# Optimization experiments

Measured on AMD Instinct MI355X. Metric: run time of the kernel, lower is better.

Reference implementation:

```python
import jax, jax.numpy as jnp
import numpy as np

EMBED = 128
HEADS = 8
PER_DIM = EMBED // HEADS


def setup_inputs() -> dict:
    key = jax.random.key(0)
    ks = jax.random.split(key, 8)
    N, T, C = 512, 32, EMBED
    values = jax.random.normal(ks[0], (N, T, C), dtype=jnp.float32)
    keys = jax.random.normal(ks[1], (N, T, C), dtype=jnp.float32)
    query = jax.random.normal(ks[2], (N, T, C), dtype=jnp.float32)
    s = 1.0 / np.sqrt(PER_DIM)
    Wq = jax.random.normal(ks[3], (PER_DIM, PER_DIM), dtype=jnp.float32) * s
    Wk = jax.random.normal(ks[4], (PER_DIM, PER_DIM), dtype=jnp.float32) * s
    Wv = jax.random.normal(ks[5], (PER_DIM, PER_DIM), dtype=jnp.float32) * s
    Wfc = jax.random.normal(ks[6], (C, C), dtype=jnp.float32) * (1.0 / np.sqrt(C))
    bfc = jax.random.normal(ks[7], (C,), dtype=jnp.float32) * 0.01
    return {"values": values, "keys": keys, "query": query, "heads": HEADS,
            "Wq": Wq, "Wk": Wk, "Wv": Wv, "Wfc": Wfc, "bfc": bfc}


def reference(values, keys, query, heads, Wq, Wk, Wv, Wfc, bfc):
    N, T, C = query.shape
    d = C // heads
    # Faithful to source bug: queries are built from `values`, not `query`.
    q = values.reshape(N, T, heads, d)
    k = keys.reshape(N, T, heads, d)
    v = values.reshape(N, T, heads, d)
    # nn.Linear (no bias): x @ W.T
    q = jnp.einsum('nthd,ed->nthe', q, Wq)
    k = jnp.einsum('nthd,ed->nthe', k, Wk)
    v = jnp.einsum('nthd,ed->nthe', v, Wv)
    # attention over the node axis: scores [q_node, k_node, t, h]
    attn = jnp.einsum('qthd,kthd->qkth', q, k)
    attention = jax.nn.softmax(attn / jnp.sqrt(jnp.float32(C)), axis=1)
    out = jnp.einsum('qkth,kthd->qthd', attention, v)
    out = out.reshape(N, T, C)
    out = jnp.einsum('ntc,ec->nte', out, Wfc) + bfc
    return out
```

## Files before the change

kernel.cpp:

```cpp
#include <hip/hip_runtime.h>

typedef __bf16 bf16x8 __attribute__((ext_vector_type(8)));
typedef float  f32x16 __attribute__((ext_vector_type(16)));

#define NN 512
#define TT 32
#define HH 8
#define CCH 128
#define RS (TT*CCH)
#define WS_U4_PER_TH 2048

__device__ __forceinline__ unsigned cvt_pk_bf16(float a, float b) {
    unsigned r;
    asm("v_cvt_pk_bf16_f32 %0, %1, %2" : "=v"(r) : "v"(a), "v"(b));
    return r;
}

__device__ __forceinline__ void permswap(unsigned& a, unsigned& b) {
    asm volatile("v_permlane32_swap_b32 %0, %1" : "+v"(a), "+v"(b));
}

__device__ __forceinline__ void split8(const float4 a, const float4 b, uint4& h, uint4& l) {
    const unsigned ax = __float_as_uint(a.x), ay = __float_as_uint(a.y);
    const unsigned az = __float_as_uint(a.z), aw = __float_as_uint(a.w);
    const unsigned bx = __float_as_uint(b.x), by = __float_as_uint(b.y);
    const unsigned bz = __float_as_uint(b.z), bw = __float_as_uint(b.w);
    h.x = (ay & 0xFFFF0000u) | (ax >> 16);
    h.y = (aw & 0xFFFF0000u) | (az >> 16);
    h.z = (by & 0xFFFF0000u) | (bx >> 16);
    h.w = (bw & 0xFFFF0000u) | (bz >> 16);
    const float lax = a.x - __uint_as_float(ax & 0xFFFF0000u);
    const float lay = a.y - __uint_as_float(ay & 0xFFFF0000u);
    const float laz = a.z - __uint_as_float(az & 0xFFFF0000u);
    const float law = a.w - __uint_as_float(aw & 0xFFFF0000u);
    const float lbx = b.x - __uint_as_float(bx & 0xFFFF0000u);
    const float lby = b.y - __uint_as_float(by & 0xFFFF0000u);
    const float lbz = b.z - __uint_as_float(bz & 0xFFFF0000u);
    const float lbw = b.w - __uint_as_float(bw & 0xFFFF0000u);
    l.x = cvt_pk_bf16(lax, lay);
    l.y = cvt_pk_bf16(laz, law);
    l.z = cvt_pk_bf16(lbx, lby);
    l.w = cvt_pk_bf16(lbz, lbw);
}

__global__ __launch_bounds__(256) void proj_kernel(
    const float* __restrict__ vals,
    const float* __restrict__ keys,
    const float* __restrict__ Wq,
    const float* __restrict__ Wk,
    const float* __restrict__ Wv,
    uint4* __restrict__ ws)
{
    __shared__ float wlds[512];
    __shared__ uint4 k2l[512];
    __shared__ uint4 vpl[512];

    const int tid  = threadIdx.x;
    const int bid  = blockIdx.x;
    const int th   = bid >> 1;
    const int half = bid & 1;
    const int t = th >> 3;
    const int h = th & 7;
    const size_t cb0 = (size_t)t*CCH + h*16;

    {
        const int d = tid >> 4, dp = tid & 15;
        float a = 0.f;
        #pragma unroll
        for (int e = 0; e < 16; ++e) a = fmaf(Wq[e*16+d], Wk[e*16+dp], a);
        wlds[tid]       = a * 0.12751744503131863f;
        wlds[256 + tid] = Wv[tid];
    }
    __syncthreads();

    const int n = half*256 + tid;
    const float* vrow = vals + (size_t)n*RS + cb0;
    const float* krow = keys + (size_t)n*RS + cb0;
    float kr[16], vr[16];
    #pragma unroll
    for (int i = 0; i < 16; i += 4) {
        *(float4*)&kr[i] = *(const float4*)(krow + i);
        *(float4*)&vr[i] = *(const float4*)(vrow + i);
    }
    float k2[16], vp[16];
    #pragma unroll
    for (int d = 0; d < 16; ++d) {
        const float4 m0 = *(const float4*)&wlds[d*16];
        const float4 m1 = *(const float4*)&wlds[d*16+4];
        const float4 m2 = *(const float4*)&wlds[d*16+8];
        const float4 m3 = *(const float4*)&wlds[d*16+12];
        const float4 w0 = *(const float4*)&wlds[256 + d*16];
        const float4 w1 = *(const float4*)&wlds[256 + d*16+4];
        const float4 w2 = *(const float4*)&wlds[256 + d*16+8];
        const float4 w3 = *(const float4*)&wlds[256 + d*16+12];
        k2[d] = kr[0]*m0.x + kr[1]*m0.y + kr[2]*m0.z + kr[3]*m0.w
              + kr[4]*m1.x + kr[5]*m1.y + kr[6]*m1.z + kr[7]*m1.w
              + kr[8]*m2.x + kr[9]*m2.y + kr[10]*m2.z + kr[11]*m2.w
              + kr[12]*m3.x + kr[13]*m3.y + kr[14]*m3.z + kr[15]*m3.w;
        vp[d] = vr[0]*w0.x + vr[1]*w0.y + vr[2]*w0.z + vr[3]*w0.w
              + vr[4]*w1.x + vr[5]*w1.y + vr[6]*w1.z + vr[7]*w1.w
              + vr[8]*w2.x + vr[9]*w2.y + vr[10]*w2.z + vr[11]*w2.w
              + vr[12]*w3.x + vr[13]*w3.y + vr[14]*w3.z + vr[15]*w3.w;
    }
    const int kt_loc = tid >> 5, r = tid & 31;
    uint4 lo4, hi4;
    lo4.x = cvt_pk_bf16(k2[0],k2[1]);   lo4.y = cvt_pk_bf16(k2[2],k2[3]);
    lo4.z = cvt_pk_bf16(k2[4],k2[5]);   lo4.w = cvt_pk_bf16(k2[6],k2[7]);
    hi4.x = cvt_pk_bf16(k2[8],k2[9]);   hi4.y = cvt_pk_bf16(k2[10],k2[11]);
    hi4.z = cvt_pk_bf16(k2[12],k2[13]); hi4.w = cvt_pk_bf16(k2[14],k2[15]);
    k2l[kt_loc*64 + r]      = lo4;
    k2l[kt_loc*64 + r + 32] = hi4;
    {
        unsigned short* vph = (unsigned short*)vpl;
        const int f_loc = kt_loc*2 + (r >> 4);
        const int lg = (r >> 3) & 1;
        const int ii = r & 7;
        #pragma unroll
        for (int e = 0; e < 16; ++e)
            vph[(size_t)(f_loc*32 + lg*16 + e)*8 + ii] =
                (unsigned short)(cvt_pk_bf16(vp[e], vp[e]) & 0xffffu);
    }
    __syncthreads();

    uint4* dk = ws + (size_t)th*WS_U4_PER_TH + half*512;
    uint4* dv = ws + (size_t)th*WS_U4_PER_TH + 1024 + half*512;
    #pragma unroll
    for (int i = 0; i < 2; ++i) {
        dk[i*256 + tid] = k2l[i*256 + tid];
        dv[i*256 + tid] = vpl[i*256 + tid];
    }
}

__global__ __launch_bounds__(256, 4) void attn_mfma(
    const float* __restrict__ vals,
    const uint4* __restrict__ ws,
    float* __restrict__ obuf)
{
    __shared__ uint4 k2f[1024];
    __shared__ uint4 vpfc[1024];
    __shared__ uint4 dummy[32];

    const int tid  = threadIdx.x;
    const int lane = tid & 63;
    const int wv   = tid >> 6;
    const int bid  = blockIdx.x;
    const int th   = bid & 255;
    const int qq   = bid >> 8;
    const int t = th >> 3;
    const int h = th & 7;
    const size_t cb0 = (size_t)t*CCH + h*16;

    const int qr = lane & 31;
    const int dh = (lane >> 5) * 8;

    const int nq = qq*128 + wv*32 + qr;
    const float* qp = vals + (size_t)nq*RS + cb0 + dh;
    const float4 qa = *(const float4*)qp;
    const float4 qb = *(const float4*)(qp + 4);

    const uint4* src = ws + (size_t)th*WS_U4_PER_TH;
    #pragma unroll
    for (int i = 0; i < 4; ++i) k2f[i*256 + tid]  = src[i*256 + tid];
    #pragma unroll
    for (int i = 0; i < 4; ++i) vpfc[i*256 + tid] = src[1024 + i*256 + tid];
    if (tid < 32) {
        const unsigned pv = (tid == 0 || tid == 16) ? 0x3F803F80u : 0u;
        dummy[tid] = make_uint4(pv, pv, pv, pv);
    }
    __syncthreads();

    bf16x8 qf;
    {
        uint4 u;
        u.x = cvt_pk_bf16(qa.x, qa.y);
        u.y = cvt_pk_bf16(qa.z, qa.w);
        u.z = cvt_pk_bf16(qb.x, qb.y);
        u.w = cvt_pk_bf16(qb.z, qb.w);
        qf = __builtin_bit_cast(bf16x8, u);
    }

    const bool vlive = (lane & 31) < 16;
    const uint4* vbase = vlive ? (vpfc + (lane & 31) + (lane >> 5)*16)
                               : (dummy + ((lane & 31) - 16) + (lane >> 5)*16);
    const int kstep = vlive ? 64 : 0;
    const int sstep = vlive ? 32 : 0;

    f32x16 zc, acc;
    #pragma unroll
    for (int r2 = 0; r2 < 16; ++r2) { zc[r2] = 0.f; acc[r2] = 0.f; }

    #pragma unroll 2
    for (int kt = 0; kt < 16; ++kt) {
        const bf16x8 ak = __builtin_bit_cast(bf16x8, k2f[kt*64 + lane]);
        const uint4 rd0 = vbase[kt*kstep];
        const uint4 rd1 = vbase[kt*kstep + sstep];

        const f32x16 s = __builtin_amdgcn_mfma_f32_32x32x16_bf16(ak, qf, zc, 0, 0, 0);
        unsigned w0 = cvt_pk_bf16(__builtin_amdgcn_exp2f(s[0]),  __builtin_amdgcn_exp2f(s[1]));
        unsigned w1 = cvt_pk_bf16(__builtin_amdgcn_exp2f(s[2]),  __builtin_amdgcn_exp2f(s[3]));
        unsigned w2 = cvt_pk_bf16(__builtin_amdgcn_exp2f(s[4]),  __builtin_amdgcn_exp2f(s[5]));
        unsigned w3 = cvt_pk_bf16(__builtin_amdgcn_exp2f(s[6]),  __builtin_amdgcn_exp2f(s[7]));
        unsigned w4 = cvt_pk_bf16(__builtin_amdgcn_exp2f(s[8]),  __builtin_amdgcn_exp2f(s[9]));
        unsigned w5 = cvt_pk_bf16(__builtin_amdgcn_exp2f(s[10]), __builtin_amdgcn_exp2f(s[11]));
        unsigned w6 = cvt_pk_bf16(__builtin_amdgcn_exp2f(s[12]), __builtin_amdgcn_exp2f(s[13]));
        unsigned w7 = cvt_pk_bf16(__builtin_amdgcn_exp2f(s[14]), __builtin_amdgcn_exp2f(s[15]));
        permswap(w0, w2);
        permswap(w1, w3);
        permswap(w4, w6);
        permswap(w5, w7);
        const uint4 pb0 = make_uint4(w0, w1, w2, w3);
        const uint4 pb1 = make_uint4(w4, w5, w6, w7);
        acc = __builtin_amdgcn_mfma_f32_32x32x16_bf16(
                  __builtin_bit_cast(bf16x8, rd0), __builtin_bit_cast(bf16x8, pb0), acc, 0, 0, 0);
        acc = __builtin_amdgcn_mfma_f32_32x32x16_bf16(
                  __builtin_bit_cast(bf16x8, rd1), __builtin_bit_cast(bf16x8, pb1), acc, 0, 0, 0);
    }

    const bool lohalf = lane < 32;
    float den = acc[8];
    const float ds = __shfl_xor(den, 32);
    if (!lohalf) den = ds;
    const float inv = 1.f / den;
    float* orow = obuf + (size_t)nq*RS + cb0 + (lohalf ? 0 : 4);
    float4 o0, o1;
    o0.x = acc[0]*inv; o0.y = acc[1]*inv; o0.z = acc[2]*inv; o0.w = acc[3]*inv;
    o1.x = acc[4]*inv; o1.y = acc[5]*inv; o1.z = acc[6]*inv; o1.w = acc[7]*inv;
    *(float4*)orow       = o0;
    *(float4*)(orow + 8) = o1;
}

__global__ __launch_bounds__(256) void fc_mfma(
    float* __restrict__ io,
    const float* __restrict__ Wfc,
    const float* __restrict__ bfc)
{
    __shared__ float xs[64 * 132];
    __shared__ uint4 whf[2048];
    __shared__ uint4 wlf[2048];

    const int tid  = threadIdx.x;
    const int lane = tid & 63;
    const int wv   = tid >> 6;
    const int rowbase = blockIdx.x * 64;

    #pragma unroll
    for (int i = 0; i < 8; ++i) {
        const int idx4 = i*256 + tid;
        const int row = idx4 >> 5, c4 = idx4 & 31;
        const float4 v = ((const float4*)(io + (size_t)rowbase*CCH))[idx4];
        *(float4*)&xs[row*132 + c4*4] = v;
    }
    #pragma unroll
    for (int i = 0; i < 8; ++i) {
        const int idx = i*256 + tid;
        const int ct = idx >> 9, ks = (idx >> 6) & 7, l = idx & 63;
        const int e = ct*32 + (l & 31);
        const int k = ks*16 + (l >> 5)*8;
        const float* wp = Wfc + (size_t)e*CCH + k;
        const float4 wa = *(const float4*)wp;
        const float4 wb = *(const float4*)(wp + 4);
        uint4 h, lo;
        split8(wa, wb, h, lo);
        whf[idx] = h;
        wlf[idx] = lo;
    }
    __syncthreads();

    const int rt  = wv & 1;
    const int ctb = (wv >> 1) * 2;
    const int xrow = rt*32 + (lane & 31);
    const int kof  = (lane >> 5) * 8;

    f32x16 acc0, acc1;
    #pragma unroll
    for (int r2 = 0; r2 < 16; ++r2) { acc0[r2] = 0.f; acc1[r2] = 0.f; }

    #pragma unroll 2
    for (int ks = 0; ks < 8; ++ks) {
        const float* xp = &xs[xrow*132 + ks*16 + kof];
        const float4 xa = *(const float4*)xp;
        const float4 xb = *(const float4*)(xp + 4);
        uint4 bh, bl;
        split8(xa, xb, bh, bl);
        const bf16x8 Bh = __builtin_bit_cast(bf16x8, bh);
        const bf16x8 Bl = __builtin_bit_cast(bf16x8, bl);
        {
            const int base = (ctb+0)*512 + ks*64 + lane;
            const bf16x8 Ah = __builtin_bit_cast(bf16x8, whf[base]);
            const bf16x8 Al = __builtin_bit_cast(bf16x8, wlf[base]);
            acc0 = __builtin_amdgcn_mfma_f32_32x32x16_bf16(Ah, Bh, acc0, 0, 0, 0);
            acc0 = __builtin_amdgcn_mfma_f32_32x32x16_bf16(Al, Bh, acc0, 0, 0, 0);
            acc0 = __builtin_amdgcn_mfma_f32_32x32x16_bf16(Ah, Bl, acc0, 0, 0, 0);
        }
        {
            const int base = (ctb+1)*512 + ks*64 + lane;
            const bf16x8 Ah = __builtin_bit_cast(bf16x8, whf[base]);
            const bf16x8 Al = __builtin_bit_cast(bf16x8, wlf[base]);
            acc1 = __builtin_amdgcn_mfma_f32_32x32x16_bf16(Ah, Bh, acc1, 0, 0, 0);
            acc1 = __builtin_amdgcn_mfma_f32_32x32x16_bf16(Al, Bh, acc1, 0, 0, 0);
            acc1 = __builtin_amdgcn_mfma_f32_32x32x16_bf16(Ah, Bl, acc1, 0, 0, 0);
        }
    }

    const int orow = rowbase + rt*32 + (lane & 31);
    const int hio  = (lane >> 5) * 4;
    #pragma unroll
    for (int c = 0; c < 2; ++c) {
        const f32x16& a = c ? acc1 : acc0;
        const int ct = ctb + c;
        #pragma unroll
        for (int g = 0; g < 4; ++g) {
            const int e0 = ct*32 + g*8 + hio;
            const float4 b = *(const float4*)&bfc[e0];
            float4 o;
            o.x = a[g*4+0] + b.x;
            o.y = a[g*4+1] + b.y;
            o.z = a[g*4+2] + b.z;
            o.w = a[g*4+3] + b.w;
            *(float4*)&io[(size_t)orow*CCH + e0] = o;
        }
    }
}

extern "C" void kernel_launch(void* const* d_in, const int* in_sizes, int n_in,
                              void* d_out, int out_size, void* d_ws, size_t ws_size,
                              hipStream_t stream)
{
    const float* vals = (const float*)d_in[0];
    const float* keys = (const float*)d_in[1];
    const float* Wq  = (const float*)d_in[4];
    const float* Wk  = (const float*)d_in[5];
    const float* Wv  = (const float*)d_in[6];
    const float* Wfc = (const float*)d_in[7];
    const float* bfc = (const float*)d_in[8];
    float* out = (float*)d_out;
    uint4* ws = (uint4*)d_ws;

    proj_kernel<<<dim3(512),  dim3(256), 0, stream>>>(vals, keys, Wq, Wk, Wv, ws);
    attn_mfma  <<<dim3(1024), dim3(256), 0, stream>>>(vals, ws, out);
    fc_mfma    <<<dim3(256),  dim3(256), 0, stream>>>(out, Wfc, bfc);
}
```

Baseline: 35.29 us.

## Coalesce projection loads via LDS staging and widen proj/fc blocks

The projection kernel now has each block cover one time step and 32 nodes, reading full contiguous 512-byte rows of keys and values into a padded LDS stage. The old per-thread 64-byte strided reads were poorly coalesced. Blocks grow to 512 threads, and the work is split so each thread computes half of the output dims for one (node, head) pair. The fc kernel also goes to 512 threads with one 32x32 tile per wave and now reads attention output from a separate workspace buffer instead of working in place. This trades extra LDS and barriers for better global memory access.

```diff
diff --git a/kernel.cpp b/kernel.cpp
--- a/kernel.cpp
+++ b/kernel.cpp
@@ -9,6 +9,7 @@
 #define CCH 128
 #define RS (TT*CCH)
 #define WS_U4_PER_TH 2048
+#define WS_OUT_OFF 524288
 
 __device__ __forceinline__ unsigned cvt_pk_bf16(float a, float b) {
     unsigned r;
@@ -43,7 +44,7 @@
     l.w = cvt_pk_bf16(lbz, lbw);
 }
 
-__global__ __launch_bounds__(256) void proj_kernel(
+__global__ __launch_bounds__(512) void proj_kernel(
     const float* __restrict__ vals,
     const float* __restrict__ keys,
     const float* __restrict__ Wq,
@@ -52,18 +53,16 @@
     uint4* __restrict__ ws)
 {
     __shared__ float wlds[512];
+    __shared__ float stage[32*164];
     __shared__ uint4 k2l[512];
     __shared__ uint4 vpl[512];
 
-    const int tid  = threadIdx.x;
-    const int bid  = blockIdx.x;
-    const int th   = bid >> 1;
-    const int half = bid & 1;
-    const int t = th >> 3;
-    const int h = th & 7;
-    const size_t cb0 = (size_t)t*CCH + h*16;
-
-    {
+    const int tid = threadIdx.x;
+    const int bid = blockIdx.x;
+    const int t = bid >> 4;
+    const int g = bid & 15;
+
+    if (tid < 256) {
         const int d = tid >> 4, dp = tid & 15;
         float a = 0.f;
         #pragma unroll
@@ -71,63 +70,88 @@
         wlds[tid]       = a * 0.12751744503131863f;
         wlds[256 + tid] = Wv[tid];
     }
-    __syncthreads();
-
-    const int n = half*256 + tid;
-    const float* vrow = vals + (size_t)n*RS + cb0;
-    const float* krow = keys + (size_t)n*RS + cb0;
-    float kr[16], vr[16];
-    #pragma unroll
-    for (int i = 0; i < 16; i += 4) {
-        *(float4*)&kr[i] = *(const float4*)(krow + i);
-        *(float4*)&vr[i] = *(const float4*)(vrow + i);
-    }
-    float k2[16], vp[16];
-    #pragma unroll
-    for (int d = 0; d < 16; ++d) {
-        const float4 m0 = *(const float4*)&wlds[d*16];
-        const float4 m1 = *(const float4*)&wlds[d*16+4];
-        const float4 m2 = *(const float4*)&wlds[d*16+8];
-        const float4 m3 = *(const float4*)&wlds[d*16+12];
-        const float4 w0 = *(const float4*)&wlds[256 + d*16];
-        const float4 w1 = *(const float4*)&wlds[256 + d*16+4];
-        const float4 w2 = *(const float4*)&wlds[256 + d*16+8];
-        const float4 w3 = *(const float4*)&wlds[256 + d*16+12];
-        k2[d] = kr[0]*m0.x + kr[1]*m0.y + kr[2]*m0.z + kr[3]*m0.w
-              + kr[4]*m1.x + kr[5]*m1.y + kr[6]*m1.z + kr[7]*m1.w
-              + kr[8]*m2.x + kr[9]*m2.y + kr[10]*m2.z + kr[11]*m2.w
-              + kr[12]*m3.x + kr[13]*m3.y + kr[14]*m3.z + kr[15]*m3.w;
-        vp[d] = vr[0]*w0.x + vr[1]*w0.y + vr[2]*w0.z + vr[3]*w0.w
-              + vr[4]*w1.x + vr[5]*w1.y + vr[6]*w1.z + vr[7]*w1.w
-              + vr[8]*w2.x + vr[9]*w2.y + vr[10]*w2.z + vr[11]*w2.w
-              + vr[12]*w3.x + vr[13]*w3.y + vr[14]*w3.z + vr[15]*w3.w;
-    }
-    const int kt_loc = tid >> 5, r = tid & 31;
-    uint4 lo4, hi4;
-    lo4.x = cvt_pk_bf16(k2[0],k2[1]);   lo4.y = cvt_pk_bf16(k2[2],k2[3]);
-    lo4.z = cvt_pk_bf16(k2[4],k2[5]);   lo4.w = cvt_pk_bf16(k2[6],k2[7]);
-    hi4.x = cvt_pk_bf16(k2[8],k2[9]);   hi4.y = cvt_pk_bf16(k2[10],k2[11]);
-    hi4.z = cvt_pk_bf16(k2[12],k2[13]); hi4.w = cvt_pk_bf16(k2[14],k2[15]);
-    k2l[kt_loc*64 + r]      = lo4;
-    k2l[kt_loc*64 + r + 32] = hi4;
+    #pragma unroll
+    for (int i = 0; i < 2; ++i) {
+        const int idx = i*512 + tid;
+        const int row = idx >> 5, c4 = idx & 31;
+        const float4 v = *(const float4*)(keys + (size_t)(g*32+row)*RS + (size_t)t*CCH + c4*4);
+        *(float4*)&stage[row*164 + (c4>>2)*20 + (c4&3)*4] = v;
+    }
+    __syncthreads();
+
+    const int u = tid & 255, dhalf = tid >> 8;
+    const int r = u >> 3, h = u & 7;
+
     {
+        float kr[16];
+        #pragma unroll
+        for (int i = 0; i < 16; i += 4)
+            *(float4*)&kr[i] = *(const float4*)&stage[r*164 + h*20 + i];
+        float k2[8];
+        #pragma unroll
+        for (int dd = 0; dd < 8; ++dd) {
+            const int d = dhalf*8 + dd;
+            const float4 m0 = *(const float4*)&wlds[d*16];
+            const float4 m1 = *(const float4*)&wlds[d*16+4];
+            const float4 m2 = *(const float4*)&wlds[d*16+8];
+            const float4 m3 = *(const float4*)&wlds[d*16+12];
+            k2[dd] = kr[0]*m0.x + kr[1]*m0.y + kr[2]*m0.z + kr[3]*m0.w
+                   + kr[4]*m1.x + kr[5]*m1.y + kr[6]*m1.z + kr[7]*m1.w
+                   + kr[8]*m2.x + kr[9]*m2.y + kr[10]*m2.z + kr[11]*m2.w
+                   + kr[12]*m3.x + kr[13]*m3.y + kr[14]*m3.z + kr[15]*m3.w;
+        }
+        uint4 p;
+        p.x = cvt_pk_bf16(k2[0],k2[1]);  p.y = cvt_pk_bf16(k2[2],k2[3]);
+        p.z = cvt_pk_bf16(k2[4],k2[5]);  p.w = cvt_pk_bf16(k2[6],k2[7]);
+        k2l[h*64 + dhalf*32 + r] = p;
+    }
+    __syncthreads();
+
+    #pragma unroll
+    for (int i = 0; i < 2; ++i) {
+        const int idx = i*512 + tid;
+        const int row = idx >> 5, c4 = idx & 31;
+        const float4 v = *(const float4*)(vals + (size_t)(g*32+row)*RS + (size_t)t*CCH + c4*4);
+        *(float4*)&stage[row*164 + (c4>>2)*20 + (c4&3)*4] = v;
+    }
+    __syncthreads();
+
+    {
+        float vr[16];
+        #pragma unroll
+        for (int i = 0; i < 16; i += 4)
+            *(float4*)&vr[i] = *(const float4*)&stage[r*164 + h*20 + i];
+        float vp[8];
+        #pragma unroll
+        for (int dd = 0; dd < 8; ++dd) {
+            const int d = dhalf*8 + dd;
+            const float4 w0 = *(const float4*)&wlds[256 + d*16];
+            const float4 w1 = *(const float4*)&wlds[256 + d*16+4];
+            const float4 w2 = *(const float4*)&wlds[256 + d*16+8];
+            const float4 w3 = *(const float4*)&wlds[256 + d*16+12];
+            vp[dd] = vr[0]*w0.x + vr[1]*w0.y + vr[2]*w0.z + vr[3]*w0.w
+                   + vr[4]*w1.x + vr[5]*w1.y + vr[6]*w1.z + vr[7]*w1.w
+                   + vr[8]*w2.x + vr[9]*w2.y + vr[10]*w2.z + vr[11]*w2.w
+                   + vr[12]*w3.x + vr[13]*w3.y + vr[14]*w3.z + vr[15]*w3.w;
+        }
         unsigned short* vph = (unsigned short*)vpl;
-        const int f_loc = kt_loc*2 + (r >> 4);
+        const int f_loc = r >> 4;
         const int lg = (r >> 3) & 1;
         const int ii = r & 7;
         #pragma unroll
-        for (int e = 0; e < 16; ++e)
-            vph[(size_t)(f_loc*32 + lg*16 + e)*8 + ii] =
-                (unsigned short)(cvt_pk_bf16(vp[e], vp[e]) & 0xffffu);
-    }
-    __syncthreads();
-
-    uint4* dk = ws + (size_t)th*WS_U4_PER_TH + half*512;
-    uint4* dv = ws + (size_t)th*WS_U4_PER_TH + 1024 + half*512;
-    #pragma unroll
-    for (int i = 0; i < 2; ++i) {
-        dk[i*256 + tid] = k2l[i*256 + tid];
-        dv[i*256 + tid] = vpl[i*256 + tid];
+        for (int dd = 0; dd < 8; ++dd) {
+            const int e = dhalf*8 + dd;
+            vph[(size_t)(h*64 + f_loc*32 + lg*16 + e)*8 + ii] =
+                (unsigned short)(cvt_pk_bf16(vp[dd], vp[dd]) & 0xffffu);
+        }
+    }
+    __syncthreads();
+
+    {
+        const int hh = tid >> 6, e = tid & 63;
+        uint4* dst = ws + (size_t)(t*8 + hh)*WS_U4_PER_TH;
+        dst[g*64 + e]        = k2l[tid];
+        dst[1024 + g*64 + e] = vpl[tid];
     }
 }
 
@@ -229,8 +253,9 @@
     *(float4*)(orow + 8) = o1;
 }
 
-__global__ __launch_bounds__(256) void fc_mfma(
-    float* __restrict__ io,
+__global__ __launch_bounds__(512) void fc_mfma(
+    const float* __restrict__ xin,
+    float* __restrict__ out,
     const float* __restrict__ Wfc,
     const float* __restrict__ bfc)
 {
@@ -244,36 +269,36 @@
     const int rowbase = blockIdx.x * 64;
 
     #pragma unroll
-    for (int i = 0; i < 8; ++i) {
-        const int idx4 = i*256 + tid;
+    for (int i = 0; i < 4; ++i) {
+        const int idx4 = i*512 + tid;
         const int row = idx4 >> 5, c4 = idx4 & 31;
-        const float4 v = ((const float4*)(io + (size_t)rowbase*CCH))[idx4];
+        const float4 v = ((const float4*)(xin + (size_t)rowbase*CCH))[idx4];
         *(float4*)&xs[row*132 + c4*4] = v;
     }
     #pragma unroll
-    for (int i = 0; i < 8; ++i) {
-        const int idx = i*256 + tid;
+    for (int i = 0; i < 4; ++i) {
+        const int idx = i*512 + tid;
         const int ct = idx >> 9, ks = (idx >> 6) & 7, l = idx & 63;
         const int e = ct*32 + (l & 31);
         const int k = ks*16 + (l >> 5)*8;
         const float* wp = Wfc + (size_t)e*CCH + k;
         const float4 wa = *(const float4*)wp;
         const float4 wb = *(const float4*)(wp + 4);
-        uint4 h, lo;
-        split8(wa, wb, h, lo);
-        whf[idx] = h;
+        uint4 hh, lo;
+        split8(wa, wb, hh, lo);
+        whf[idx] = hh;
         wlf[idx] = lo;
     }
     __syncthreads();
 
-    const int rt  = wv & 1;
-    const int ctb = (wv >> 1) * 2;
+    const int rt = wv >> 2;
+    const int ct = wv & 3;
     const int xrow = rt*32 + (lane & 31);
     const int kof  = (lane >> 5) * 8;
 
-    f32x16 acc0, acc1;
-    #pragma unroll
-    for (int r2 = 0; r2 < 16; ++r2) { acc0[r2] = 0.f; acc1[r2] = 0.f; }
+    f32x16 acc;
+    #pragma unroll
+    for (int r2 = 0; r2 < 16; ++r2) acc[r2] = 0.f;
 
     #pragma unroll 2
     for (int ks = 0; ks < 8; ++ks) {
@@ -284,41 +309,26 @@
         split8(xa, xb, bh, bl);
         const bf16x8 Bh = __builtin_bit_cast(bf16x8, bh);
         const bf16x8 Bl = __builtin_bit_cast(bf16x8, bl);
-        {
-            const int base = (ctb+0)*512 + ks*64 + lane;
-            const bf16x8 Ah = __builtin_bit_cast(bf16x8, whf[base]);
-            const bf16x8 Al = __builtin_bit_cast(bf16x8, wlf[base]);
-            acc0 = __builtin_amdgcn_mfma_f32_32x32x16_bf16(Ah, Bh, acc0, 0, 0, 0);
-            acc0 = __builtin_amdgcn_mfma_f32_32x32x16_bf16(Al, Bh, acc0, 0, 0, 0);
-            acc0 = __builtin_amdgcn_mfma_f32_32x32x16_bf16(Ah, Bl, acc0, 0, 0, 0);
-        }
-        {
-            const int base = (ctb+1)*512 + ks*64 + lane;
-            const bf16x8 Ah = __builtin_bit_cast(bf16x8, whf[base]);
-            const bf16x8 Al = __builtin_bit_cast(bf16x8, wlf[base]);
-            acc1 = __builtin_amdgcn_mfma_f32_32x32x16_bf16(Ah, Bh, acc1, 0, 0, 0);
-            acc1 = __builtin_amdgcn_mfma_f32_32x32x16_bf16(Al, Bh, acc1, 0, 0, 0);
-            acc1 = __builtin_amdgcn_mfma_f32_32x32x16_bf16(Ah, Bl, acc1, 0, 0, 0);
-        }
+        const int base = ct*512 + ks*64 + lane;
+        const bf16x8 Ah = __builtin_bit_cast(bf16x8, whf[base]);
+        const bf16x8 Al = __builtin_bit_cast(bf16x8, wlf[base]);
+        acc = __builtin_amdgcn_mfma_f32_32x32x16_bf16(Ah, Bh, acc, 0, 0, 0);
+        acc = __builtin_amdgcn_mfma_f32_32x32x16_bf16(Al, Bh, acc, 0, 0, 0);
+        acc = __builtin_amdgcn_mfma_f32_32x32x16_bf16(Ah, Bl, acc, 0, 0, 0);
     }
 
     const int orow = rowbase + rt*32 + (lane & 31);
     const int hio  = (lane >> 5) * 4;
     #pragma unroll
-    for (int c = 0; c < 2; ++c) {
-        const f32x16& a = c ? acc1 : acc0;
-        const int ct = ctb + c;
-        #pragma unroll
-        for (int g = 0; g < 4; ++g) {
-            const int e0 = ct*32 + g*8 + hio;
-            const float4 b = *(const float4*)&bfc[e0];
-            float4 o;
-            o.x = a[g*4+0] + b.x;
-            o.y = a[g*4+1] + b.y;
-            o.z = a[g*4+2] + b.z;
-            o.w = a[g*4+3] + b.w;
-            *(float4*)&io[(size_t)orow*CCH + e0] = o;
-        }
+    for (int g = 0; g < 4; ++g) {
+        const int e0 = ct*32 + g*8 + hio;
+        const float4 b = *(const float4*)&bfc[e0];
+        float4 o;
+        o.x = acc[g*4+0] + b.x;
+        o.y = acc[g*4+1] + b.y;
+        o.z = acc[g*4+2] + b.z;
+        o.w = acc[g*4+3] + b.w;
+        *(float4*)&out[(size_t)orow*CCH + e0] = o;
     }
 }
 
@@ -335,8 +345,9 @@
     const float* bfc = (const float*)d_in[8];
     float* out = (float*)d_out;
     uint4* ws = (uint4*)d_ws;
-
-    proj_kernel<<<dim3(512),  dim3(256), 0, stream>>>(vals, keys, Wq, Wk, Wv, ws);
-    attn_mfma  <<<dim3(1024), dim3(256), 0, stream>>>(vals, ws, out);
-    fc_mfma    <<<dim3(256),  dim3(256), 0, stream>>>(out, Wfc, bfc);
-}
+    float* wsout = (float*)(ws + WS_OUT_OFF);
+
+    proj_kernel<<<dim3(512),  dim3(512), 0, stream>>>(vals, keys, Wq, Wk, Wv, ws);
+    attn_mfma  <<<dim3(1024), dim3(256), 0, stream>>>(vals, ws, wsout);
+    fc_mfma    <<<dim3(256),  dim3(512), 0, stream>>>(wsout, out, Wfc, bfc);
+}
```

Measured after the change: 33.17 us. 1.06x faster.
